# Optimization experiments

Hardware: AMD Instinct MI355X
Metric: run time of the kernel (lower is better)

Reference implementation:

```python
import jax, jax.numpy as jnp
import numpy as np

INPUT_NDIMS = 1024
HIDDEN = 512
LATENT = 50
BATCH = 16384

def setup_inputs() -> dict:
    key = jax.random.key(0)
    ks = jax.random.split(key, 12)
    s = 0.02
    x = jax.random.uniform(ks[0], (BATCH, INPUT_NDIMS), dtype=jnp.float32)
    u = 0.01 + 0.98 * jax.random.uniform(ks[1], (BATCH, LATENT), dtype=jnp.float32)
    W1 = s * jax.random.normal(ks[2], (HIDDEN, INPUT_NDIMS), dtype=jnp.float32)
    b1 = jnp.zeros((HIDDEN,), jnp.float32)
    Wa = s * jax.random.normal(ks[3], (LATENT, HIDDEN), dtype=jnp.float32)
    ba = jnp.zeros((LATENT,), jnp.float32)
    Wb = s * jax.random.normal(ks[4], (LATENT, HIDDEN), dtype=jnp.float32)
    bb = jnp.zeros((LATENT,), jnp.float32)
    W2 = s * jax.random.normal(ks[5], (HIDDEN, LATENT), dtype=jnp.float32)
    b2 = jnp.zeros((HIDDEN,), jnp.float32)
    W3 = s * jax.random.normal(ks[6], (INPUT_NDIMS, HIDDEN), dtype=jnp.float32)
    b3 = jnp.zeros((INPUT_NDIMS,), jnp.float32)
    return dict(x=x, u=u, W1=W1, b1=b1, Wa=Wa, ba=ba, Wb=Wb, bb=bb, W2=W2, b2=b2, W3=W3, b3=b3)

def _stick_segments(v):
    # pi[:, k] = v[:, k] * prod_{j<k} (1 - v[:, j])  -- single O(K) cumprod pass
    cp = jnp.cumprod(1.0 - v, axis=1)                       # inclusive cumprod
    excl = jnp.concatenate([jnp.ones_like(cp[:, :1]), cp[:, :-1]], axis=1)
    return v * excl

def reference(x, u, W1, b1, Wa, ba, Wb, bb, W2, b2, W3, b3):
    # encoder: MLP -> positive Kumaraswamy params alpha (param1), beta (param2)
    h = jax.nn.relu(x @ W1.T + b1)                           # [B, H]
    alpha = jax.nn.softplus(h @ Wa.T + ba) + 1e-4            # [B, K]
    beta = jax.nn.softplus(h @ Wb.T + bb) + 1e-4             # [B, K]
    # Kumaraswamy reparameterized sample: v = (1 - u^(1/beta))^(1/alpha)
    v = jnp.power(1.0 - jnp.power(u, 1.0 / beta), 1.0 / alpha)
    # set_v_K_to_one: force last stick fraction to 1 so segments sum to 1
    v = v.at[:, -1].set(1.0)
    pi = _stick_segments(v)                                  # [B, K], rows sum to 1
    # decoder: MLP with sigmoid output
    h2 = jax.nn.relu(pi @ W2.T + b2)                         # [B, H]
    recon = jax.nn.sigmoid(h2 @ W3.T + b3)                   # [B, D]
    return recon, alpha, beta
```

## Files before the change

### kernel.cpp

```cpp
#include <hip/hip_runtime.h>
#include <hip/hip_bf16.h>

typedef __hip_bfloat16 bf16_t;
typedef __attribute__((ext_vector_type(4))) float f32x4;
typedef __attribute__((ext_vector_type(8))) __bf16 bf16x8;
typedef __attribute__((ext_vector_type(8))) short s16x8;
typedef __attribute__((ext_vector_type(4))) unsigned short u16x4;

#define BATCH 16384
#define NDIM  1024
#define HID   512
#define LAT   50

#define LOG2E 1.44269504088896340736f
#define RLOG2E 0.69314718055994530942f

__device__ __forceinline__ float ex2(float x) { return __builtin_amdgcn_exp2f(x); }
__device__ __forceinline__ float lg2(float x) { return __builtin_amdgcn_logf(x); }
__device__ __forceinline__ float rcp(float x) { return __builtin_amdgcn_rcpf(x); }

__device__ inline unsigned short f2b_u(float f) {
  union { bf16_t b; unsigned short u; } cv; cv.b = __float2bfloat16(f); return cv.u;
}

__device__ __forceinline__ void gload16(const void* src, void* dst_lds) {
  __builtin_amdgcn_global_load_lds(
      reinterpret_cast<const __attribute__((address_space(1))) void*>(
          reinterpret_cast<unsigned long long>(src)),
      reinterpret_cast<__attribute__((address_space(3))) void*>(
          static_cast<unsigned>(reinterpret_cast<unsigned long long>(dst_lds))),
      16, 0, 0);
}

__global__ void prep_w_kernel(const float* __restrict__ W1, const float* __restrict__ W3,
                              const float* __restrict__ Wa, const float* __restrict__ Wb,
                              const float* __restrict__ W2, const float* __restrict__ ba,
                              const float* __restrict__ bb,
                              bf16_t* __restrict__ w1, bf16_t* __restrict__ w3,
                              bf16_t* __restrict__ wab, bf16_t* __restrict__ w2p,
                              float* __restrict__ bab)
{
  const int W1U  = (HID * NDIM) / 4;
  const int W3U  = (NDIM * HID) / 4;
  const int WABN = 128 * HID;
  const int W2PN = HID * 64;
  const int TOT  = W1U + W3U + WABN + W2PN + 128;
  for (int i = blockIdx.x * blockDim.x + threadIdx.x; i < TOT;
       i += gridDim.x * blockDim.x) {
    int j = i;
    if (j < W1U) {
      const f32x4 v = ((const f32x4*)W1)[j];
      u16x4 o; o[0]=f2b_u(v[0]); o[1]=f2b_u(v[1]); o[2]=f2b_u(v[2]); o[3]=f2b_u(v[3]);
      ((u16x4*)w1)[j] = o; continue;
    }
    j -= W1U;
    if (j < W3U) {
      const f32x4 v = ((const f32x4*)W3)[j];
      u16x4 o; o[0]=f2b_u(v[0]); o[1]=f2b_u(v[1]); o[2]=f2b_u(v[2]); o[3]=f2b_u(v[3]);
      ((u16x4*)w3)[j] = o; continue;
    }
    j -= W3U;
    if (j < WABN) {
      const int n = j >> 9, k = j & 511;
      float v = (n < 50) ? Wa[n * 512 + k] : ((n < 100) ? Wb[(n - 50) * 512 + k] : 0.f);
      wab[j] = __float2bfloat16(v); continue;
    }
    j -= WABN;
    if (j < W2PN) {
      const int n = j >> 6, k = j & 63;
      w2p[j] = __float2bfloat16(k < 50 ? W2[n * 50 + k] : 0.f); continue;
    }
    j -= W2PN;
    bab[j] = (j < 50) ? ba[j] : ((j < 100) ? bb[j - 50] : 0.f);
  }
}

template<int A_F32, int EPI, int MT, int DB>
__global__ __launch_bounds__(512, 4)
void gemm_kernel(const void* __restrict__ Av, const bf16_t* __restrict__ B,
                 const float* __restrict__ bias, void* __restrict__ out0,
                 float* __restrict__ out_a, float* __restrict__ out_b,
                 int M, int N, int K)
{
  constexpr int MI  = MT / 32;
  constexpr int IA  = MT / 64;
  constexpr int BUF = MT * 128 + 16384;
  __shared__ char lds[(DB ? 2 : 1) * BUF];

  const int tid  = threadIdx.x;
  const int swzid = ((blockIdx.x & 7) * (gridDim.x >> 3)) + (blockIdx.x >> 3);
  const int nblocks = N >> 7;
  const int bn   = swzid % nblocks;
  const int bm   = swzid / nblocks;
  const int wid  = tid >> 6;
  const int lane = tid & 63;
  const int l15  = lane & 15;
  const int l4   = lane >> 4;
  const int wm   = (wid >> 2) * (MT / 2);
  const int wn   = (wid & 3) << 5;
  const int uw   = __builtin_amdgcn_readfirstlane(wid);

  f32x4 acc[MI][2] = {};
  f32x4 areg[2 * IA];

  auto stage_B = [&](char* buf, int k0) {
    char* lB = buf + MT * 128;
    #pragma unroll
    for (int i = 0; i < 2; ++i) {
      const int c  = (i * 8 + uw) * 64 + lane;
      const int r  = c >> 3;
      const int sp = c & 7;
      const int sl = sp ^ (r & 7);
      gload16(B + (size_t)(bn * 128 + r) * K + k0 + sl * 8,
              lB + (i * 8 + uw) * 1024);
    }
  };
  auto stage_A_bf16 = [&](char* buf, int k0) {
    const bf16_t* A = (const bf16_t*)Av;
    #pragma unroll
    for (int i = 0; i < IA; ++i) {
      const int c  = (i * 8 + uw) * 64 + lane;
      const int r  = c >> 3;
      const int sp = c & 7;
      const int sl = sp ^ (r & 7);
      gload16(A + (size_t)(bm * MT + r) * K + k0 + sl * 8,
              buf + (i * 8 + uw) * 1024);
    }
  };
  auto load_A_f32 = [&](int k0) {
    const float* A = (const float*)Av;
    #pragma unroll
    for (int i = 0; i < IA; ++i) {
      const int c  = i * 512 + tid;
      const int r  = c >> 3;
      const int sl = c & 7;
      const float* s = A + (size_t)(bm * MT + r) * K + k0 + sl * 8;
      areg[2 * i]     = *(const f32x4*)s;
      areg[2 * i + 1] = *(const f32x4*)(s + 4);
    }
  };
  auto write_A_f32 = [&](char* buf) {
    #pragma unroll
    for (int i = 0; i < IA; ++i) {
      const int c  = i * 512 + tid;
      const int r  = c >> 3;
      const int sl = c & 7;
      const int sp = sl ^ (r & 7);
      union { s16x8 v; unsigned short us[8]; } o;
      const f32x4 v0 = areg[2 * i], v1 = areg[2 * i + 1];
      o.us[0]=f2b_u(v0[0]); o.us[1]=f2b_u(v0[1]); o.us[2]=f2b_u(v0[2]); o.us[3]=f2b_u(v0[3]);
      o.us[4]=f2b_u(v1[0]); o.us[5]=f2b_u(v1[1]); o.us[6]=f2b_u(v1[2]); o.us[7]=f2b_u(v1[3]);
      *(s16x8*)(buf + r * 128 + sp * 16) = o.v;
    }
  };
  auto compute = [&](const char* buf) {
    const char* lA = buf;
    const char* lB = buf + MT * 128;
    #pragma unroll
    for (int h = 0; h < 2; ++h) {
      bf16x8 af[MI], bfr[2];
      #pragma unroll
      for (int mi = 0; mi < MI; ++mi) {
        const int row = wm + mi * 16 + l15;
        const int sp  = (h * 4 + l4) ^ (row & 7);
        af[mi] = *(const bf16x8*)(lA + row * 128 + sp * 16);
      }
      #pragma unroll
      for (int ni = 0; ni < 2; ++ni) {
        const int row = wn + ni * 16 + l15;
        const int sp  = (h * 4 + l4) ^ (row & 7);
        bfr[ni] = *(const bf16x8*)(lB + row * 128 + sp * 16);
      }
      #pragma unroll
      for (int mi = 0; mi < MI; ++mi)
        #pragma unroll
        for (int ni = 0; ni < 2; ++ni)
          acc[mi][ni] = __builtin_amdgcn_mfma_f32_16x16x32_bf16(
              af[mi], bfr[ni], acc[mi][ni], 0, 0, 0);
    }
  };

  const int nt = K >> 6;
  if (A_F32) { load_A_f32(0); write_A_f32(lds); }
  else       { stage_A_bf16(lds, 0); }
  stage_B(lds, 0);
  __syncthreads();

  int cur = 0;
  for (int t = 0; t < nt - 1; ++t) {
    char* nbuf = lds + (DB ? (cur ^ 1) * BUF : 0);
    const int k0n = (t + 1) << 6;
    if (A_F32) load_A_f32(k0n);
    else       stage_A_bf16(nbuf, k0n);
    stage_B(nbuf, k0n);
    compute(lds + cur * BUF);
    if (A_F32) write_A_f32(nbuf);
    __syncthreads();
    cur ^= 1;
  }
  compute(lds + cur * BUF);

  #pragma unroll
  for (int ni = 0; ni < 2; ++ni) {
    const int n  = bn * 128 + wn + ni * 16 + l15;
    const float bv = bias[n];
    #pragma unroll
    for (int mi = 0; mi < MI; ++mi) {
      #pragma unroll
      for (int r = 0; r < 4; ++r) {
        const int m  = bm * MT + wm + mi * 16 + l4 * 4 + r;
        const float t = acc[mi][ni][r] + bv;
        if (EPI == 2) {
          if (n < 100) {
            const float y =
                (t > 20.f ? t : lg2(1.f + ex2(t * LOG2E)) * RLOG2E) + 1e-4f;
            if (n < 50) out_a[(size_t)m * 50 + n] = y;
            else        out_b[(size_t)m * 50 + (n - 50)] = y;
          }
        } else if (EPI == 0) {
          ((bf16_t*)out0)[(size_t)m * N + n] = __float2bfloat16(fmaxf(t, 0.f));
        } else {
          ((float*)out0)[(size_t)m * N + n] = rcp(1.f + ex2(-t * LOG2E));
        }
      }
    }
  }
}

__global__ void stick_kernel(const float* __restrict__ u,
                             const float* __restrict__ alpha,
                             const float* __restrict__ beta,
                             bf16_t* __restrict__ pi)
{
  const int gw   = (blockIdx.x * blockDim.x + threadIdx.x) >> 6;
  const int lane = threadIdx.x & 63;
  if (gw >= BATCH) return;
  const size_t row = (size_t)gw;

  float v = 1.f, t = 1.f;
  if (lane < 49) {
    const float a  = alpha[row * 50 + lane];
    const float b  = beta[row * 50 + lane];
    const float uu = u[row * 50 + lane];
    const float tb = ex2(lg2(uu) * rcp(b));
    v = ex2(lg2(1.f - tb) * rcp(a));
    t = 1.f - v;
  }
  float p = t;
  #pragma unroll
  for (int d = 1; d < 64; d <<= 1) {
    const float o = __shfl_up(p, d, 64);
    if (lane >= d) p *= o;
  }
  float e = __shfl_up(p, 1, 64);
  if (lane == 0) e = 1.f;
  pi[row * 64 + lane] = __float2bfloat16(lane < 50 ? v * e : 0.f);
}

extern "C" void kernel_launch(void* const* d_in, const int* in_sizes, int n_in,
                              void* d_out, int out_size, void* d_ws, size_t ws_size,
                              hipStream_t stream)
{
  const float* x  = (const float*)d_in[0];
  const float* u  = (const float*)d_in[1];
  const float* W1 = (const float*)d_in[2];
  const float* b1 = (const float*)d_in[3];
  const float* Wa = (const float*)d_in[4];
  const float* ba = (const float*)d_in[5];
  const float* Wb = (const float*)d_in[6];
  const float* bb = (const float*)d_in[7];
  const float* W2 = (const float*)d_in[8];
  const float* b2 = (const float*)d_in[9];
  const float* W3 = (const float*)d_in[10];
  const float* b3 = (const float*)d_in[11];

  float* recon  = (float*)d_out;
  float* oalpha = recon + (size_t)BATCH * NDIM;
  float* obeta  = oalpha + (size_t)BATCH * LAT;

  char* ws = (char*)d_ws;
  bf16_t* h   = (bf16_t*)(ws);
  bf16_t* h2  = (bf16_t*)(ws + 16777216);
  bf16_t* pi  = (bf16_t*)(ws + 33554432);
  bf16_t* w1  = (bf16_t*)(ws + 35651584);
  bf16_t* w3  = (bf16_t*)(ws + 36700160);
  bf16_t* wab = (bf16_t*)(ws + 37748736);
  bf16_t* w2p = (bf16_t*)(ws + 37879808);
  float*  bab = (float*)(ws + 37945344);

  prep_w_kernel<<<512, 256, 0, stream>>>(W1, W3, Wa, Wb, W2, ba, bb,
                                         w1, w3, wab, w2p, bab);
  gemm_kernel<1, 0, 128, 1><<<512, 512, 0, stream>>>(
      x, w1, b1, (void*)h, nullptr, nullptr, BATCH, HID, NDIM);
  gemm_kernel<0, 2, 64, 1><<<256, 512, 0, stream>>>(
      h, wab, bab, nullptr, oalpha, obeta, BATCH, 128, HID);
  stick_kernel<<<4096, 256, 0, stream>>>(u, oalpha, obeta, pi);
  gemm_kernel<0, 0, 64, 0><<<1024, 512, 0, stream>>>(
      pi, w2p, b2, (void*)h2, nullptr, nullptr, BATCH, HID, 64);
  gemm_kernel<0, 1, 128, 1><<<1024, 512, 0, stream>>>(
      h2, w3, b3, (void*)recon, nullptr, nullptr, BATCH, NDIM, HID);
}
```

Before: 85.16 us.

## Use full-N-width 64x512 tiles for the first and last GEMMs

Adds a GEMM kernel whose block covers 64 rows by 512 columns, so each A row tile (the float32 x input, or h2) is read once per 512 output columns rather than once per 128. It is used for the encoder first layer and the decoder output layer, and the older kernel is trimmed to the bf16-A paths that remain. In exchange it drops double buffering (single LDS buffer with two syncs per k-step), uses 72KB of LDS per block and launches fewer blocks, which may lower occupancy and latency hiding.

```diff
diff --git a/kernel.cpp b/kernel.cpp
--- a/kernel.cpp
+++ b/kernel.cpp
@@ -75,9 +75,118 @@
   }
 }
 
-template<int A_F32, int EPI, int MT, int DB>
+template<int A_F32, int EPI>
 __global__ __launch_bounds__(512, 4)
-void gemm_kernel(const void* __restrict__ Av, const bf16_t* __restrict__ B,
+void gemm_fn_kernel(const void* __restrict__ Av, const bf16_t* __restrict__ B,
+                    const float* __restrict__ bias, void* __restrict__ out0,
+                    int M, int N, int K)
+{
+  __shared__ char lds[64 * 128 + 512 * 128];
+  char* lA = lds;
+  char* lB = lds + 8192;
+
+  const int tid  = threadIdx.x;
+  const int swzid = ((blockIdx.x & 7) * (gridDim.x >> 3)) + (blockIdx.x >> 3);
+  const int nbn  = N >> 9;
+  const int bn   = swzid % nbn;
+  const int bm   = swzid / nbn;
+  const int wid  = tid >> 6;
+  const int lane = tid & 63;
+  const int l15  = lane & 15;
+  const int l4   = lane >> 4;
+  const int uw   = __builtin_amdgcn_readfirstlane(wid);
+
+  f32x4 acc[4][4] = {};
+  f32x4 areg[2];
+
+  const int nt = K >> 6;
+  for (int t = 0; t < nt; ++t) {
+    const int k0 = t << 6;
+    if (A_F32) {
+      const float* A = (const float*)Av;
+      const int r  = tid >> 3;
+      const int sl = tid & 7;
+      const float* s = A + (size_t)(bm * 64 + r) * K + k0 + sl * 8;
+      areg[0] = *(const f32x4*)s;
+      areg[1] = *(const f32x4*)(s + 4);
+    }
+    if (t) __syncthreads();
+    if (A_F32) {
+      const int r  = tid >> 3;
+      const int sl = tid & 7;
+      const int sp = sl ^ (r & 7);
+      union { s16x8 v; unsigned short us[8]; } o;
+      o.us[0]=f2b_u(areg[0][0]); o.us[1]=f2b_u(areg[0][1]);
+      o.us[2]=f2b_u(areg[0][2]); o.us[3]=f2b_u(areg[0][3]);
+      o.us[4]=f2b_u(areg[1][0]); o.us[5]=f2b_u(areg[1][1]);
+      o.us[6]=f2b_u(areg[1][2]); o.us[7]=f2b_u(areg[1][3]);
+      *(s16x8*)(lA + r * 128 + sp * 16) = o.v;
+    } else {
+      const bf16_t* A = (const bf16_t*)Av;
+      const int c  = tid;
+      const int r  = c >> 3;
+      const int sp = c & 7;
+      const int sl = sp ^ (r & 7);
+      gload16(A + (size_t)(bm * 64 + r) * K + k0 + sl * 8, lA + uw * 1024);
+    }
+    #pragma unroll
+    for (int i = 0; i < 8; ++i) {
+      const int c  = (i * 8 + uw) * 64 + lane;
+      const int r  = c >> 3;
+      const int sp = c & 7;
+      const int sl = sp ^ (r & 7);
+      gload16(B + (size_t)(bn * 512 + r) * K + k0 + sl * 8,
+              lB + (i * 8 + uw) * 1024);
+    }
+    __syncthreads();
+
+    #pragma unroll
+    for (int h = 0; h < 2; ++h) {
+      bf16x8 af[4], bfr[4];
+      #pragma unroll
+      for (int mi = 0; mi < 4; ++mi) {
+        const int row = mi * 16 + l15;
+        const int sp  = (h * 4 + l4) ^ (row & 7);
+        af[mi] = *(const bf16x8*)(lA + row * 128 + sp * 16);
+      }
+      #pragma unroll
+      for (int ni = 0; ni < 4; ++ni) {
+        const int row = wid * 64 + ni * 16 + l15;
+        const int sp  = (h * 4 + l4) ^ (row & 7);
+        bfr[ni] = *(const bf16x8*)(lB + row * 128 + sp * 16);
+      }
+      #pragma unroll
+      for (int mi = 0; mi < 4; ++mi)
+        #pragma unroll
+        for (int ni = 0; ni < 4; ++ni)
+          acc[mi][ni] = __builtin_amdgcn_mfma_f32_16x16x32_bf16(
+              af[mi], bfr[ni], acc[mi][ni], 0, 0, 0);
+    }
+  }
+
+  #pragma unroll
+  for (int ni = 0; ni < 4; ++ni) {
+    const int n  = bn * 512 + wid * 64 + ni * 16 + l15;
+    const float bv = bias[n];
+    #pragma unroll
+    for (int mi = 0; mi < 4; ++mi) {
+      #pragma unroll
+      for (int r = 0; r < 4; ++r) {
+        const int m  = bm * 64 + mi * 16 + l4 * 4 + r;
+        const float t = acc[mi][ni][r] + bv;
+        if (EPI == 0) {
+          ((bf16_t*)out0)[(size_t)m * N + n] = __float2bfloat16(fmaxf(t, 0.f));
+        } else {
+          ((float*)out0)[(size_t)m * N + n] = rcp(1.f + ex2(-t * LOG2E));
+        }
+      }
+    }
+  }
+}
+
+template<int EPI, int MT, int DB>
+__global__ __launch_bounds__(512, 4)
+void gemm_kernel(const bf16_t* __restrict__ A, const bf16_t* __restrict__ B,
                  const float* __restrict__ bias, void* __restrict__ out0,
                  float* __restrict__ out_a, float* __restrict__ out_b,
                  int M, int N, int K)
@@ -101,7 +210,6 @@
   const int uw   = __builtin_amdgcn_readfirstlane(wid);
 
   f32x4 acc[MI][2] = {};
-  f32x4 areg[2 * IA];
 
   auto stage_B = [&](char* buf, int k0) {
     char* lB = buf + MT * 128;
@@ -115,8 +223,7 @@
               lB + (i * 8 + uw) * 1024);
     }
   };
-  auto stage_A_bf16 = [&](char* buf, int k0) {
-    const bf16_t* A = (const bf16_t*)Av;
+  auto stage_A = [&](char* buf, int k0) {
     #pragma unroll
     for (int i = 0; i < IA; ++i) {
       const int c  = (i * 8 + uw) * 64 + lane;
@@ -127,32 +234,6 @@
               buf + (i * 8 + uw) * 1024);
     }
   };
-  auto load_A_f32 = [&](int k0) {
-    const float* A = (const float*)Av;
-    #pragma unroll
-    for (int i = 0; i < IA; ++i) {
-      const int c  = i * 512 + tid;
-      const int r  = c >> 3;
-      const int sl = c & 7;
-      const float* s = A + (size_t)(bm * MT + r) * K + k0 + sl * 8;
-      areg[2 * i]     = *(const f32x4*)s;
-      areg[2 * i + 1] = *(const f32x4*)(s + 4);
-    }
-  };
-  auto write_A_f32 = [&](char* buf) {
-    #pragma unroll
-    for (int i = 0; i < IA; ++i) {
-      const int c  = i * 512 + tid;
-      const int r  = c >> 3;
-      const int sl = c & 7;
-      const int sp = sl ^ (r & 7);
-      union { s16x8 v; unsigned short us[8]; } o;
-      const f32x4 v0 = areg[2 * i], v1 = areg[2 * i + 1];
-      o.us[0]=f2b_u(v0[0]); o.us[1]=f2b_u(v0[1]); o.us[2]=f2b_u(v0[2]); o.us[3]=f2b_u(v0[3]);
-      o.us[4]=f2b_u(v1[0]); o.us[5]=f2b_u(v1[1]); o.us[6]=f2b_u(v1[2]); o.us[7]=f2b_u(v1[3]);
-      *(s16x8*)(buf + r * 128 + sp * 16) = o.v;
-    }
-  };
   auto compute = [&](const char* buf) {
     const char* lA = buf;
     const char* lB = buf + MT * 128;
@@ -181,8 +262,7 @@
   };
 
   const int nt = K >> 6;
-  if (A_F32) { load_A_f32(0); write_A_f32(lds); }
-  else       { stage_A_bf16(lds, 0); }
+  stage_A(lds, 0);
   stage_B(lds, 0);
   __syncthreads();
 
@@ -190,11 +270,9 @@
   for (int t = 0; t < nt - 1; ++t) {
     char* nbuf = lds + (DB ? (cur ^ 1) * BUF : 0);
     const int k0n = (t + 1) << 6;
-    if (A_F32) load_A_f32(k0n);
-    else       stage_A_bf16(nbuf, k0n);
+    stage_A(nbuf, k0n);
     stage_B(nbuf, k0n);
     compute(lds + cur * BUF);
-    if (A_F32) write_A_f32(nbuf);
     __syncthreads();
     cur ^= 1;
   }
@@ -217,10 +295,8 @@
             if (n < 50) out_a[(size_t)m * 50 + n] = y;
             else        out_b[(size_t)m * 50 + (n - 50)] = y;
           }
-        } else if (EPI == 0) {
+        } else {
           ((bf16_t*)out0)[(size_t)m * N + n] = __float2bfloat16(fmaxf(t, 0.f));
-        } else {
-          ((float*)out0)[(size_t)m * N + n] = rcp(1.f + ex2(-t * LOG2E));
         }
       }
     }
@@ -290,13 +366,13 @@
 
   prep_w_kernel<<<512, 256, 0, stream>>>(W1, W3, Wa, Wb, W2, ba, bb,
                                          w1, w3, wab, w2p, bab);
-  gemm_kernel<1, 0, 128, 1><<<512, 512, 0, stream>>>(
-      x, w1, b1, (void*)h, nullptr, nullptr, BATCH, HID, NDIM);
-  gemm_kernel<0, 2, 64, 1><<<256, 512, 0, stream>>>(
+  gemm_fn_kernel<1, 0><<<256, 512, 0, stream>>>(
+      x, w1, b1, (void*)h, BATCH, HID, NDIM);
+  gemm_kernel<2, 64, 1><<<256, 512, 0, stream>>>(
       h, wab, bab, nullptr, oalpha, obeta, BATCH, 128, HID);
   stick_kernel<<<4096, 256, 0, stream>>>(u, oalpha, obeta, pi);
-  gemm_kernel<0, 0, 64, 0><<<1024, 512, 0, stream>>>(
+  gemm_kernel<0, 64, 0><<<1024, 512, 0, stream>>>(
       pi, w2p, b2, (void*)h2, nullptr, nullptr, BATCH, HID, 64);
-  gemm_kernel<0, 1, 128, 1><<<1024, 512, 0, stream>>>(
-      h2, w3, b3, (void*)recon, nullptr, nullptr, BATCH, NDIM, HID);
-}
+  gemm_fn_kernel<0, 1><<<512, 512, 0, stream>>>(
+      h2, w3, b3, (void*)recon, BATCH, NDIM, HID);
+}
```

Result: slower. 102.7 us (+20.6%).

## Pre-convert x to bf16 in prep kernel and fuse stick-breaking into alpha/beta GEMM

Applied to the files above, without the earlier changes.

Converts the input x to bf16 in the prep kernel so the first GEMM can stage A asynchronously via global_load_lds instead of a register load-convert-store path. The stick-breaking computation is fused into the alpha/beta GEMM epilogue using LDS, removing a separate kernel launch and the re-read of alpha/beta. The trade-off is an extra full pass over x (fp32 read, bf16 write and reread) plus extra LDS syncs in the epilogue.

```diff
diff --git a/kernel.cpp b/kernel.cpp
--- a/kernel.cpp
+++ b/kernel.cpp
@@ -32,22 +32,29 @@
       16, 0, 0);
 }
 
-__global__ void prep_w_kernel(const float* __restrict__ W1, const float* __restrict__ W3,
-                              const float* __restrict__ Wa, const float* __restrict__ Wb,
-                              const float* __restrict__ W2, const float* __restrict__ ba,
-                              const float* __restrict__ bb,
-                              bf16_t* __restrict__ w1, bf16_t* __restrict__ w3,
-                              bf16_t* __restrict__ wab, bf16_t* __restrict__ w2p,
-                              float* __restrict__ bab)
+__global__ void prep_kernel(const float* __restrict__ x,  const float* __restrict__ W1,
+                            const float* __restrict__ W3, const float* __restrict__ Wa,
+                            const float* __restrict__ Wb, const float* __restrict__ W2,
+                            const float* __restrict__ ba, const float* __restrict__ bb,
+                            bf16_t* __restrict__ xb,  bf16_t* __restrict__ w1,
+                            bf16_t* __restrict__ w3,  bf16_t* __restrict__ wab,
+                            bf16_t* __restrict__ w2p, float* __restrict__ bab)
 {
+  const int XU   = (BATCH * NDIM) / 4;
   const int W1U  = (HID * NDIM) / 4;
   const int W3U  = (NDIM * HID) / 4;
   const int WABN = 128 * HID;
   const int W2PN = HID * 64;
-  const int TOT  = W1U + W3U + WABN + W2PN + 128;
+  const int TOT  = XU + W1U + W3U + WABN + W2PN + 128;
   for (int i = blockIdx.x * blockDim.x + threadIdx.x; i < TOT;
        i += gridDim.x * blockDim.x) {
     int j = i;
+    if (j < XU) {
+      const f32x4 v = ((const f32x4*)x)[j];
+      u16x4 o; o[0]=f2b_u(v[0]); o[1]=f2b_u(v[1]); o[2]=f2b_u(v[2]); o[3]=f2b_u(v[3]);
+      ((u16x4*)xb)[j] = o; continue;
+    }
+    j -= XU;
     if (j < W1U) {
       const f32x4 v = ((const f32x4*)W1)[j];
       u16x4 o; o[0]=f2b_u(v[0]); o[1]=f2b_u(v[1]); o[2]=f2b_u(v[2]); o[3]=f2b_u(v[3]);
@@ -75,17 +82,19 @@
   }
 }
 
-template<int A_F32, int EPI, int MT, int DB>
+template<int EPI, int MT, int DB, int STICK>
 __global__ __launch_bounds__(512, 4)
-void gemm_kernel(const void* __restrict__ Av, const bf16_t* __restrict__ B,
+void gemm_kernel(const bf16_t* __restrict__ A, const bf16_t* __restrict__ B,
                  const float* __restrict__ bias, void* __restrict__ out0,
                  float* __restrict__ out_a, float* __restrict__ out_b,
+                 const float* __restrict__ u, bf16_t* __restrict__ pi,
                  int M, int N, int K)
 {
   constexpr int MI  = MT / 32;
   constexpr int IA  = MT / 64;
   constexpr int BUF = MT * 128 + 16384;
-  __shared__ char lds[(DB ? 2 : 1) * BUF];
+  constexpr int LDSZ = (DB ? 2 : 1) * BUF;
+  __shared__ char lds[STICK ? (LDSZ > 26624 ? LDSZ : 26624) : LDSZ];
 
   const int tid  = threadIdx.x;
   const int swzid = ((blockIdx.x & 7) * (gridDim.x >> 3)) + (blockIdx.x >> 3);
@@ -101,7 +110,6 @@
   const int uw   = __builtin_amdgcn_readfirstlane(wid);
 
   f32x4 acc[MI][2] = {};
-  f32x4 areg[2 * IA];
 
   auto stage_B = [&](char* buf, int k0) {
     char* lB = buf + MT * 128;
@@ -115,8 +123,7 @@
               lB + (i * 8 + uw) * 1024);
     }
   };
-  auto stage_A_bf16 = [&](char* buf, int k0) {
-    const bf16_t* A = (const bf16_t*)Av;
+  auto stage_A = [&](char* buf, int k0) {
     #pragma unroll
     for (int i = 0; i < IA; ++i) {
       const int c  = (i * 8 + uw) * 64 + lane;
@@ -127,32 +134,6 @@
               buf + (i * 8 + uw) * 1024);
     }
   };
-  auto load_A_f32 = [&](int k0) {
-    const float* A = (const float*)Av;
-    #pragma unroll
-    for (int i = 0; i < IA; ++i) {
-      const int c  = i * 512 + tid;
-      const int r  = c >> 3;
-      const int sl = c & 7;
-      const float* s = A + (size_t)(bm * MT + r) * K + k0 + sl * 8;
-      areg[2 * i]     = *(const f32x4*)s;
-      areg[2 * i + 1] = *(const f32x4*)(s + 4);
-    }
-  };
-  auto write_A_f32 = [&](char* buf) {
-    #pragma unroll
-    for (int i = 0; i < IA; ++i) {
-      const int c  = i * 512 + tid;
-      const int r  = c >> 3;
-      const int sl = c & 7;
-      const int sp = sl ^ (r & 7);
-      union { s16x8 v; unsigned short us[8]; } o;
-      const f32x4 v0 = areg[2 * i], v1 = areg[2 * i + 1];
-      o.us[0]=f2b_u(v0[0]); o.us[1]=f2b_u(v0[1]); o.us[2]=f2b_u(v0[2]); o.us[3]=f2b_u(v0[3]);
-      o.us[4]=f2b_u(v1[0]); o.us[5]=f2b_u(v1[1]); o.us[6]=f2b_u(v1[2]); o.us[7]=f2b_u(v1[3]);
-      *(s16x8*)(buf + r * 128 + sp * 16) = o.v;
-    }
-  };
   auto compute = [&](const char* buf) {
     const char* lA = buf;
     const char* lB = buf + MT * 128;
@@ -181,8 +162,7 @@
   };
 
   const int nt = K >> 6;
-  if (A_F32) { load_A_f32(0); write_A_f32(lds); }
-  else       { stage_A_bf16(lds, 0); }
+  stage_A(lds, 0);
   stage_B(lds, 0);
   __syncthreads();
 
@@ -190,15 +170,16 @@
   for (int t = 0; t < nt - 1; ++t) {
     char* nbuf = lds + (DB ? (cur ^ 1) * BUF : 0);
     const int k0n = (t + 1) << 6;
-    if (A_F32) load_A_f32(k0n);
-    else       stage_A_bf16(nbuf, k0n);
+    stage_A(nbuf, k0n);
     stage_B(nbuf, k0n);
     compute(lds + cur * BUF);
-    if (A_F32) write_A_f32(nbuf);
     __syncthreads();
     cur ^= 1;
   }
   compute(lds + cur * BUF);
+
+  float* sm = (float*)lds;
+  if (STICK) __syncthreads();
 
   #pragma unroll
   for (int ni = 0; ni < 2; ++ni) {
@@ -208,7 +189,8 @@
     for (int mi = 0; mi < MI; ++mi) {
       #pragma unroll
       for (int r = 0; r < 4; ++r) {
-        const int m  = bm * MT + wm + mi * 16 + l4 * 4 + r;
+        const int ml = wm + mi * 16 + l4 * 4 + r;
+        const int m  = bm * MT + ml;
         const float t = acc[mi][ni][r] + bv;
         if (EPI == 2) {
           if (n < 100) {
@@ -216,6 +198,7 @@
                 (t > 20.f ? t : lg2(1.f + ex2(t * LOG2E)) * RLOG2E) + 1e-4f;
             if (n < 50) out_a[(size_t)m * 50 + n] = y;
             else        out_b[(size_t)m * 50 + (n - 50)] = y;
+            if (STICK) sm[ml * 104 + n + (n < 50 ? 0 : 2)] = y;
           }
         } else if (EPI == 0) {
           ((bf16_t*)out0)[(size_t)m * N + n] = __float2bfloat16(fmaxf(t, 0.f));
@@ -225,36 +208,33 @@
       }
     }
   }
-}
-
-__global__ void stick_kernel(const float* __restrict__ u,
-                             const float* __restrict__ alpha,
-                             const float* __restrict__ beta,
-                             bf16_t* __restrict__ pi)
-{
-  const int gw   = (blockIdx.x * blockDim.x + threadIdx.x) >> 6;
-  const int lane = threadIdx.x & 63;
-  if (gw >= BATCH) return;
-  const size_t row = (size_t)gw;
-
-  float v = 1.f, t = 1.f;
-  if (lane < 49) {
-    const float a  = alpha[row * 50 + lane];
-    const float b  = beta[row * 50 + lane];
-    const float uu = u[row * 50 + lane];
-    const float tb = ex2(lg2(uu) * rcp(b));
-    v = ex2(lg2(1.f - tb) * rcp(a));
-    t = 1.f - v;
-  }
-  float p = t;
-  #pragma unroll
-  for (int d = 1; d < 64; d <<= 1) {
-    const float o = __shfl_up(p, d, 64);
-    if (lane >= d) p *= o;
-  }
-  float e = __shfl_up(p, 1, 64);
-  if (lane == 0) e = 1.f;
-  pi[row * 64 + lane] = __float2bfloat16(lane < 50 ? v * e : 0.f);
+
+  if (STICK) {
+    __syncthreads();
+    #pragma unroll 1
+    for (int rr = 0; rr < 8; ++rr) {
+      const int rl = wid * 8 + rr;
+      const size_t m = (size_t)(bm * MT + rl);
+      float v = 1.f, t = 1.f;
+      if (lane < 49) {
+        const float a  = sm[rl * 104 + lane];
+        const float b  = sm[rl * 104 + 52 + lane];
+        const float uu = u[m * 50 + lane];
+        const float tb = ex2(lg2(uu) * rcp(b));
+        v = ex2(lg2(1.f - tb) * rcp(a));
+        t = 1.f - v;
+      }
+      float p = t;
+      #pragma unroll
+      for (int d = 1; d < 64; d <<= 1) {
+        const float o = __shfl_up(p, d, 64);
+        if (lane >= d) p *= o;
+      }
+      float e = __shfl_up(p, 1, 64);
+      if (lane == 0) e = 1.f;
+      pi[m * 64 + lane] = __float2bfloat16(lane < 50 ? v * e : 0.f);
+    }
+  }
 }
 
 extern "C" void kernel_launch(void* const* d_in, const int* in_sizes, int n_in,
@@ -279,24 +259,27 @@
   float* obeta  = oalpha + (size_t)BATCH * LAT;
 
   char* ws = (char*)d_ws;
-  bf16_t* h   = (bf16_t*)(ws);
-  bf16_t* h2  = (bf16_t*)(ws + 16777216);
-  bf16_t* pi  = (bf16_t*)(ws + 33554432);
-  bf16_t* w1  = (bf16_t*)(ws + 35651584);
-  bf16_t* w3  = (bf16_t*)(ws + 36700160);
-  bf16_t* wab = (bf16_t*)(ws + 37748736);
-  bf16_t* w2p = (bf16_t*)(ws + 37879808);
-  float*  bab = (float*)(ws + 37945344);
-
-  prep_w_kernel<<<512, 256, 0, stream>>>(W1, W3, Wa, Wb, W2, ba, bb,
-                                         w1, w3, wab, w2p, bab);
-  gemm_kernel<1, 0, 128, 1><<<512, 512, 0, stream>>>(
-      x, w1, b1, (void*)h, nullptr, nullptr, BATCH, HID, NDIM);
-  gemm_kernel<0, 2, 64, 1><<<256, 512, 0, stream>>>(
-      h, wab, bab, nullptr, oalpha, obeta, BATCH, 128, HID);
-  stick_kernel<<<4096, 256, 0, stream>>>(u, oalpha, obeta, pi);
-  gemm_kernel<0, 0, 64, 0><<<1024, 512, 0, stream>>>(
-      pi, w2p, b2, (void*)h2, nullptr, nullptr, BATCH, HID, 64);
-  gemm_kernel<0, 1, 128, 1><<<1024, 512, 0, stream>>>(
-      h2, w3, b3, (void*)recon, nullptr, nullptr, BATCH, NDIM, HID);
-}
+  bf16_t* xb  = (bf16_t*)(ws);
+  bf16_t* h2  = (bf16_t*)(ws);
+  bf16_t* pi  = (bf16_t*)(ws + 16777216);
+  bf16_t* h   = (bf16_t*)(ws + 33554432);
+  bf16_t* w1  = (bf16_t*)(ws + 50331648);
+  bf16_t* w3  = (bf16_t*)(ws + 51380224);
+  bf16_t* wab = (bf16_t*)(ws + 52428800);
+  bf16_t* w2p = (bf16_t*)(ws + 52559872);
+  float*  bab = (float*)(ws + 52625408);
+
+  prep_kernel<<<2048, 256, 0, stream>>>(x, W1, W3, Wa, Wb, W2, ba, bb,
+                                        xb, w1, w3, wab, w2p, bab);
+  gemm_kernel<0, 128, 1, 0><<<512, 512, 0, stream>>>(
+      xb, w1, b1, (void*)h, nullptr, nullptr, nullptr, nullptr,
+      BATCH, HID, NDIM);
+  gemm_kernel<2, 64, 1, 1><<<256, 512, 0, stream>>>(
+      h, wab, bab, nullptr, oalpha, obeta, u, pi, BATCH, 128, HID);
+  gemm_kernel<0, 64, 0, 0><<<1024, 512, 0, stream>>>(
+      pi, w2p, b2, (void*)h2, nullptr, nullptr, nullptr, nullptr,
+      BATCH, HID, 64);
+  gemm_kernel<1, 128, 1, 0><<<1024, 512, 0, stream>>>(
+      h2, w3, b3, (void*)recon, nullptr, nullptr, nullptr, nullptr,
+      BATCH, NDIM, HID);
+}
```

After: 87.19 us. +2.4%, slower.
